# Kernel optimization log

Measured on AMD Instinct MI355X. Metric: run time of the kernel, lower is better.

The kernel has to match this reference:

```python
import jax, jax.numpy as jnp
import numpy as np

N_NODES = 50000
N_EDGES = 800000
D = 64
NUM_GRAPHS = 64


def gcn_conv(x, src, dst, deg_inv_sqrt, W, b):
    # GCNConv: h = X W; out_i = sum_{j->i} norm_ij * h_j + self-loop term + b
    h = x @ W  # [N, D_out]
    norm = deg_inv_sqrt[src] * deg_inv_sqrt[dst]  # [E]
    msgs = h[src] * norm[:, None]  # [E, D_out] -- dominant gather
    out = jax.ops.segment_sum(msgs, dst, num_segments=N_NODES)
    # self-loop edge (i,i) with norm = deg_i^-1
    out = out + h * (deg_inv_sqrt ** 2)[:, None]
    return out + b


def setup_inputs() -> dict:
    key = jax.random.key(0)
    ks = jax.random.split(key, 12)
    x = jax.random.normal(ks[0], (N_NODES, D), dtype=jnp.float32)
    edge_index = jax.random.randint(ks[1], (2, N_EDGES), 0, N_NODES, dtype=jnp.int64)
    batch = jnp.sort(jax.random.randint(ks[2], (N_NODES,), 0, NUM_GRAPHS, dtype=jnp.int64))
    s = 1.0 / np.sqrt(D)
    W1 = jax.random.uniform(ks[3], (D, D), jnp.float32, -s, s)
    b1 = jnp.zeros((D,), jnp.float32)
    W2 = jax.random.uniform(ks[4], (D, D), jnp.float32, -s, s)
    b2 = jnp.zeros((D,), jnp.float32)
    W3 = jax.random.uniform(ks[5], (D, D), jnp.float32, -s, s)
    b3 = jnp.zeros((D,), jnp.float32)
    Wl = jax.random.uniform(ks[6], (D, 1), jnp.float32, -s, s)
    bl = jnp.zeros((1,), jnp.float32)
    return {"x": x, "edge_index": edge_index, "batch": batch,
            "W1": W1, "b1": b1, "W2": W2, "b2": b2, "W3": W3, "b3": b3,
            "Wl": Wl, "bl": bl}


def reference(x, edge_index, batch, W1, b1, W2, b2, W3, b3, Wl, bl):
    src, dst = edge_index[0], edge_index[1]
    # symmetric GCN normalization with self-loops: deg_i = in_degree_i + 1
    deg = jax.ops.segment_sum(jnp.ones((N_EDGES,), x.dtype), dst, num_segments=N_NODES) + 1.0
    deg_inv_sqrt = deg ** -0.5
    h = jax.nn.relu(gcn_conv(x, src, dst, deg_inv_sqrt, W1, b1))
    h = jax.nn.relu(gcn_conv(h, src, dst, deg_inv_sqrt, W2, b2))
    h = jax.nn.relu(gcn_conv(h, src, dst, deg_inv_sqrt, W3, b3))
    # global mean pool over graphs
    sums = jax.ops.segment_sum(h, batch, num_segments=NUM_GRAPHS)  # [G, D]
    counts = jax.ops.segment_sum(jnp.ones((N_NODES,), h.dtype), batch, num_segments=NUM_GRAPHS)
    pooled = sums / jnp.clip(counts, 1.0)[:, None]
    return pooled @ Wl + bl  # [G, 1]
```

## Files before the change

kernel.cpp:

```cpp
#include <hip/hip_runtime.h>

#define N_NODES 50000
#define N_EDGES 800000
#define DIM 64
#define NUM_GRAPHS 64
#define NPART 8
#define PART_NODES 6250

typedef unsigned short u16;
typedef unsigned int u32;

__device__ __forceinline__ u16 bf16_rne(float f) {
  u32 u = __float_as_uint(f);
  u32 r = (u + 0x7fffu + ((u >> 16) & 1u)) >> 16;
  return (u16)r;
}

__global__ void init_kernel(int* __restrict__ cnt, float* __restrict__ partial,
                            const float* __restrict__ x, u16* __restrict__ xh) {
  int i = blockIdx.x * blockDim.x + threadIdx.x;
  if (i < N_NODES) cnt[i] = 0;
  if (i < NUM_GRAPHS) partial[i] = 0.f;
  int stride = gridDim.x * blockDim.x;
  for (int k = i; k < N_NODES * DIM / 4; k += stride) {
    float4 v = reinterpret_cast<const float4*>(x)[k];
    ushort4 o;
    o.x = bf16_rne(v.x); o.y = bf16_rne(v.y);
    o.z = bf16_rne(v.z); o.w = bf16_rne(v.w);
    reinterpret_cast<ushort4*>(xh)[k] = o;
  }
}

__global__ void count_deg_kernel(const int* __restrict__ dst, int* __restrict__ cnt, int E) {
  int stride = gridDim.x * blockDim.x;
  for (int e = blockIdx.x * blockDim.x + threadIdx.x; e < E; e += stride)
    atomicAdd(&cnt[dst[e]], 1);
}

__global__ void scanA_kernel(const int* __restrict__ cnt, int* __restrict__ rowptr,
                             int* __restrict__ bsum, float* __restrict__ dis, int N) {
  __shared__ int wsum[16];
  int i = blockIdx.x * 1024 + threadIdx.x;
  int lane = threadIdx.x & 63, wid = threadIdx.x >> 6;
  int v = (i < N) ? cnt[i] : 0;
  if (i < N) dis[i] = rsqrtf((float)(v + 1));
  int sv = v;
  #pragma unroll
  for (int off = 1; off < 64; off <<= 1) {
    int t = __shfl_up(sv, off, 64);
    if (lane >= off) sv += t;
  }
  if (lane == 63) wsum[wid] = sv;
  __syncthreads();
  if (wid == 0) {
    int wv = (lane < 16) ? wsum[lane] : 0;
    #pragma unroll
    for (int off = 1; off < 16; off <<= 1) {
      int t = __shfl_up(wv, off, 64);
      if (lane >= off) wv += t;
    }
    if (lane < 16) wsum[lane] = wv;
  }
  __syncthreads();
  if (i < N) rowptr[i] = (wid ? wsum[wid - 1] : 0) + (sv - v);
  if (threadIdx.x == 1023) bsum[blockIdx.x] = wsum[15];
}

__global__ void scanC_kernel(int* __restrict__ rowptr, const int* __restrict__ bsum,
                             int* __restrict__ cursor, int nb, int N) {
  __shared__ int s_off;
  __shared__ int s_total;
  int b = blockIdx.x;
  if (threadIdx.x < 64) {
    int t = threadIdx.x;
    int v = (t < nb) ? bsum[t] : 0;
    #pragma unroll
    for (int off = 1; off < 64; off <<= 1) {
      int u = __shfl_up(v, off, 64);
      if (t >= off) v += u;
    }
    if (t == (b == 0 ? 0 : b - 1)) s_off = (b == 0) ? 0 : v;
    if (t == nb - 1) s_total = v;
  }
  __syncthreads();
  int i = b * 1024 + threadIdx.x;
  if (i < N) {
    int r = rowptr[i] + s_off;
    rowptr[i] = r;
    cursor[i] = r;
  }
  if (b == 0 && threadIdx.x == 0) rowptr[N] = s_total;
}

__global__ void fill_kernel(const int* __restrict__ src, const int* __restrict__ dst,
                            const float* __restrict__ dis,
                            int* __restrict__ cursor, int2* __restrict__ epair, int E) {
  int p = blockIdx.x & 7;
  int lo = p * PART_NODES, hi = lo + PART_NODES;
  int stride = (gridDim.x >> 3) * blockDim.x;
  for (int e = (blockIdx.x >> 3) * blockDim.x + threadIdx.x; e < E; e += stride) {
    int d = dst[e];
    if (d >= lo && d < hi) {
      int s = src[e];
      int pos = atomicAdd(&cursor[d], 1);
      epair[pos] = make_int2(s, __float_as_int(dis[s]));
    }
  }
}

#define UNPACK_FMA(q, d)                                              \
  a0 = fmaf(__uint_as_float((q).x << 16), (d), a0);                   \
  a1 = fmaf(__uint_as_float((q).x & 0xffff0000u), (d), a1);           \
  a2 = fmaf(__uint_as_float((q).y << 16), (d), a2);                   \
  a3 = fmaf(__uint_as_float((q).y & 0xffff0000u), (d), a3);           \
  a4 = fmaf(__uint_as_float((q).z << 16), (d), a4);                   \
  a5 = fmaf(__uint_as_float((q).z & 0xffff0000u), (d), a5);           \
  a6 = fmaf(__uint_as_float((q).w << 16), (d), a6);                   \
  a7 = fmaf(__uint_as_float((q).w & 0xffff0000u), (d), a7);

__global__ __launch_bounds__(256) void aggregate_kernel(const u16* __restrict__ Fh,
    const int* __restrict__ rowptr, const int2* __restrict__ epair,
    const float* __restrict__ dis, float* __restrict__ A, int N) {
  int node = blockIdx.x * 4 + (threadIdx.x >> 6);
  if (node >= N) return;
  int lane = threadIdx.x & 63;
  int qc = lane & 7;
  int qe = lane >> 3;
  const uint4* __restrict__ F8 = reinterpret_cast<const uint4*>(Fh);
  int beg = rowptr[node], end = rowptr[node + 1];
  float a0 = 0.f, a1 = 0.f, a2 = 0.f, a3 = 0.f;
  float a4 = 0.f, a5 = 0.f, a6 = 0.f, a7 = 0.f;
  int j = beg;
  for (; j + 16 <= end; j += 16) {
    int2 p0 = epair[j + qe];
    int2 p1 = epair[j + 8 + qe];
    uint4 q0 = F8[(size_t)p0.x * 8 + qc];
    uint4 q1 = F8[(size_t)p1.x * 8 + qc];
    float d0 = __int_as_float(p0.y), d1 = __int_as_float(p1.y);
    UNPACK_FMA(q0, d0)
    UNPACK_FMA(q1, d1)
  }
  if (j + 8 <= end) {
    int2 p0 = epair[j + qe];
    uint4 q0 = F8[(size_t)p0.x * 8 + qc];
    float d0 = __int_as_float(p0.y);
    UNPACK_FMA(q0, d0)
    j += 8;
  }
  if (j + qe < end) {
    int2 p0 = epair[j + qe];
    uint4 q0 = F8[(size_t)p0.x * 8 + qc];
    float d0 = __int_as_float(p0.y);
    UNPACK_FMA(q0, d0)
  }
  #pragma unroll
  for (int m = 8; m < 64; m <<= 1) {
    a0 += __shfl_xor(a0, m, 64); a1 += __shfl_xor(a1, m, 64);
    a2 += __shfl_xor(a2, m, 64); a3 += __shfl_xor(a3, m, 64);
    a4 += __shfl_xor(a4, m, 64); a5 += __shfl_xor(a5, m, 64);
    a6 += __shfl_xor(a6, m, 64); a7 += __shfl_xor(a7, m, 64);
  }
  if (qe == 0) {
    float dn = dis[node];
    uint4 qs = F8[(size_t)node * 8 + qc];
    float s0 = __uint_as_float(qs.x << 16), s1 = __uint_as_float(qs.x & 0xffff0000u);
    float s2 = __uint_as_float(qs.y << 16), s3 = __uint_as_float(qs.y & 0xffff0000u);
    float s4 = __uint_as_float(qs.z << 16), s5 = __uint_as_float(qs.z & 0xffff0000u);
    float s6 = __uint_as_float(qs.w << 16), s7 = __uint_as_float(qs.w & 0xffff0000u);
    float4 o0, o1;
    o0.x = (a0 + s0 * dn) * dn; o0.y = (a1 + s1 * dn) * dn;
    o0.z = (a2 + s2 * dn) * dn; o0.w = (a3 + s3 * dn) * dn;
    o1.x = (a4 + s4 * dn) * dn; o1.y = (a5 + s5 * dn) * dn;
    o1.z = (a6 + s6 * dn) * dn; o1.w = (a7 + s7 * dn) * dn;
    float4* A4 = reinterpret_cast<float4*>(A + (size_t)node * DIM + qc * 8);
    A4[0] = o0;
    A4[1] = o1;
  }
}

__global__ __launch_bounds__(256) void gemm_bias_relu(const float* __restrict__ X,
    const float* __restrict__ W, const float* __restrict__ b,
    u16* __restrict__ Fh, int N) {
  __shared__ float4 Xs[64][16];
  int col = threadIdx.x & 63, wid = threadIdx.x >> 6;
  float wreg[DIM];
  #pragma unroll
  for (int k = 0; k < DIM; ++k) wreg[k] = W[k * DIM + col];
  float bias = b[col];
  int row0 = blockIdx.x * 64;
  for (int i = threadIdx.x; i < 64 * 16; i += 256) {
    int r = i >> 4, c = i & 15;
    int gr = row0 + r;
    Xs[r][c] = (gr < N) ? reinterpret_cast<const float4*>(X)[(size_t)gr * 16 + c]
                        : make_float4(0.f, 0.f, 0.f, 0.f);
  }
  __syncthreads();
  for (int rr = 0; rr < 16; ++rr) {
    int lr = wid * 16 + rr;
    int row = row0 + lr;
    if (row >= N) break;
    float a0 = 0.f, a1 = 0.f, a2 = 0.f, a3 = 0.f;
    #pragma unroll
    for (int kk = 0; kk < 16; ++kk) {
      float4 xv = Xs[lr][kk];
      a0 = fmaf(xv.x, wreg[4 * kk + 0], a0);
      a1 = fmaf(xv.y, wreg[4 * kk + 1], a1);
      a2 = fmaf(xv.z, wreg[4 * kk + 2], a2);
      a3 = fmaf(xv.w, wreg[4 * kk + 3], a3);
    }
    float v = fmaxf(a0 + a1 + a2 + a3 + bias, 0.f);
    Fh[(size_t)row * DIM + col] = bf16_rne(v);
  }
}

__global__ __launch_bounds__(256) void gemm_dot_kernel(const float* __restrict__ X,
    const float* __restrict__ W, const float* __restrict__ b, const float* __restrict__ Wl,
    const int* __restrict__ batch, float* __restrict__ partial, int N) {
  __shared__ float4 Xs[64][16];
  __shared__ float yv[64];
  __shared__ float gpart[NUM_GRAPHS];
  int col = threadIdx.x & 63, wid = threadIdx.x >> 6;
  float wreg[DIM];
  #pragma unroll
  for (int k = 0; k < DIM; ++k) wreg[k] = W[k * DIM + col];
  float bias = b[col];
  float wl = Wl[col];
  int row0 = blockIdx.x * 64;
  if (threadIdx.x < 64) { yv[threadIdx.x] = 0.f; gpart[threadIdx.x] = 0.f; }
  for (int i = threadIdx.x; i < 64 * 16; i += 256) {
    int r = i >> 4, c = i & 15;
    int gr = row0 + r;
    Xs[r][c] = (gr < N) ? reinterpret_cast<const float4*>(X)[(size_t)gr * 16 + c]
                        : make_float4(0.f, 0.f, 0.f, 0.f);
  }
  __syncthreads();
  for (int rr = 0; rr < 16; ++rr) {
    int lr = wid * 16 + rr;
    int row = row0 + lr;
    if (row >= N) break;
    float a0 = 0.f, a1 = 0.f, a2 = 0.f, a3 = 0.f;
    #pragma unroll
    for (int kk = 0; kk < 16; ++kk) {
      float4 xv = Xs[lr][kk];
      a0 = fmaf(xv.x, wreg[4 * kk + 0], a0);
      a1 = fmaf(xv.y, wreg[4 * kk + 1], a1);
      a2 = fmaf(xv.z, wreg[4 * kk + 2], a2);
      a3 = fmaf(xv.w, wreg[4 * kk + 3], a3);
    }
    float v = fmaxf(a0 + a1 + a2 + a3 + bias, 0.f);
    float y = v * wl;
    #pragma unroll
    for (int off = 32; off > 0; off >>= 1) y += __shfl_down(y, off, 64);
    if (col == 0) yv[lr] = y;
  }
  __syncthreads();
  if (threadIdx.x < 64) {
    int row = row0 + threadIdx.x;
    if (row < N) atomicAdd(&gpart[batch[row]], yv[threadIdx.x]);
  }
  __syncthreads();
  if (threadIdx.x < NUM_GRAPHS) {
    int glo = batch[row0];
    int ghi = batch[min(row0 + 63, N - 1)];
    int g = threadIdx.x;
    if (g >= glo && g <= ghi) atomicAdd(&partial[g], gpart[g]);
  }
}

__global__ void pool_final_kernel(const float* __restrict__ partial, const int* __restrict__ batch,
                                  const float* __restrict__ bl, float* __restrict__ out, int N) {
  int g = threadIdx.x;
  int lo = 0, hi = N;
  while (lo < hi) { int m = (lo + hi) >> 1; if (batch[m] < g) lo = m + 1; else hi = m; }
  int start = lo;
  hi = N;
  while (lo < hi) { int m = (lo + hi) >> 1; if (batch[m] < g + 1) lo = m + 1; else hi = m; }
  float c = fmaxf((float)(lo - start), 1.f);
  out[g] = partial[g] / c + bl[0];
}

extern "C" void kernel_launch(void* const* d_in, const int* in_sizes, int n_in,
                              void* d_out, int out_size, void* d_ws, size_t ws_size,
                              hipStream_t stream) {
  const float* x     = (const float*)d_in[0];
  const int*   ei    = (const int*)d_in[1];
  const int*   batch = (const int*)d_in[2];
  const float* W1 = (const float*)d_in[3];
  const float* b1 = (const float*)d_in[4];
  const float* W2 = (const float*)d_in[5];
  const float* b2 = (const float*)d_in[6];
  const float* W3 = (const float*)d_in[7];
  const float* b3 = (const float*)d_in[8];
  const float* Wl = (const float*)d_in[9];
  const float* bl = (const float*)d_in[10];
  float* out = (float*)d_out;

  const int* srcp = ei;
  const int* dstp = ei + N_EDGES;

  char* ws = (char*)d_ws;
  size_t off = 0;
  auto alloc = [&](size_t bytes) { void* p = ws + off; off += (bytes + 255) & ~(size_t)255; return p; };
  int*   cnt     = (int*)  alloc((size_t)N_NODES * 4);
  float* dis     = (float*)alloc((size_t)N_NODES * 4);
  int*   rowptr  = (int*)  alloc((size_t)(N_NODES + 1) * 4);
  int*   bsum    = (int*)  alloc(64 * 4);
  float* partial = (float*)alloc(NUM_GRAPHS * 4);
  int2*  epair   = (int2*) alloc((size_t)N_EDGES * 8);
  u16*   xh      = (u16*)  alloc((size_t)N_NODES * DIM * 2);
  u16*   fh      = (u16*)  alloc((size_t)N_NODES * DIM * 2);
  float* A       = (float*)alloc((size_t)N_NODES * DIM * 4);

  const int NB = (N_NODES + 1023) / 1024;

  init_kernel<<<(N_NODES + 255) / 256, 256, 0, stream>>>(cnt, partial, x, xh);
  count_deg_kernel<<<1024, 256, 0, stream>>>(dstp, cnt, N_EDGES);
  scanA_kernel<<<NB, 1024, 0, stream>>>(cnt, rowptr, bsum, dis, N_NODES);
  scanC_kernel<<<NB, 1024, 0, stream>>>(rowptr, bsum, cnt, NB, N_NODES);
  fill_kernel<<<1024, 256, 0, stream>>>(srcp, dstp, dis, cnt, epair, N_EDGES);

  const int GB = (N_NODES + 63) / 64;
  const int AB = (N_NODES + 3) / 4;
  aggregate_kernel<<<AB, 256, 0, stream>>>(xh, rowptr, epair, dis, A, N_NODES);
  gemm_bias_relu<<<GB, 256, 0, stream>>>(A, W1, b1, fh, N_NODES);
  aggregate_kernel<<<AB, 256, 0, stream>>>(fh, rowptr, epair, dis, A, N_NODES);
  gemm_bias_relu<<<GB, 256, 0, stream>>>(A, W2, b2, xh, N_NODES);
  aggregate_kernel<<<AB, 256, 0, stream>>>(xh, rowptr, epair, dis, A, N_NODES);
  gemm_dot_kernel<<<GB, 256, 0, stream>>>(A, W3, b3, Wl, batch, partial, N_NODES);
  pool_final_kernel<<<1, 64, 0, stream>>>(partial, batch, bl, out, N_NODES);
}
```

Before: 227.0 us.

## Fuse GCN aggregation with dense transform per layer and pool via per-node outputs

Each layer's neighbour aggregation and 64x64 GEMM + bias + ReLU now run in one kernel. The aggregated row goes into a per-wave shared-memory buffer and is multiplied by W held in LDS, so the fp32 intermediate matrix is never written to or read back from global memory. The last layer writes one scalar per node (the dot with Wl), and a per-graph block reduction replaces the atomic partial sums. In exchange every block of four nodes reloads the full 16KB weight matrix into LDS, which adds heavy L2 traffic and LDS pressure that may reduce occupancy.

New measurement: 240.7 us. 1.06x slower.

```diff
diff --git a/kernel.cpp b/kernel.cpp
--- a/kernel.cpp
+++ b/kernel.cpp
@@ -16,11 +16,10 @@
   return (u16)r;
 }
 
-__global__ void init_kernel(int* __restrict__ cnt, float* __restrict__ partial,
+__global__ void init_kernel(int* __restrict__ cnt,
                             const float* __restrict__ x, u16* __restrict__ xh) {
   int i = blockIdx.x * blockDim.x + threadIdx.x;
   if (i < N_NODES) cnt[i] = 0;
-  if (i < NUM_GRAPHS) partial[i] = 0.f;
   int stride = gridDim.x * blockDim.x;
   for (int k = i; k < N_NODES * DIM / 4; k += stride) {
     float4 v = reinterpret_cast<const float4*>(x)[k];
@@ -118,15 +117,30 @@
   a6 = fmaf(__uint_as_float((q).w << 16), (d), a6);                   \
   a7 = fmaf(__uint_as_float((q).w & 0xffff0000u), (d), a7);
 
-__global__ __launch_bounds__(256) void aggregate_kernel(const u16* __restrict__ Fh,
+template <int LAST>
+__global__ __launch_bounds__(256) void fused_layer(const u16* __restrict__ Fh,
     const int* __restrict__ rowptr, const int2* __restrict__ epair,
-    const float* __restrict__ dis, float* __restrict__ A, int N) {
-  int node = blockIdx.x * 4 + (threadIdx.x >> 6);
+    const float* __restrict__ dis, const float* __restrict__ W,
+    const float* __restrict__ b, u16* __restrict__ FhOut,
+    const float* __restrict__ Wl, float* __restrict__ ynode, int N) {
+  __shared__ float Ws[DIM][DIM];
+  __shared__ float rowbuf[4][DIM];
+
+  for (int i = threadIdx.x; i < DIM * DIM / 4; i += 256)
+    reinterpret_cast<float4*>(&Ws[0][0])[i] = reinterpret_cast<const float4*>(W)[i];
+  __syncthreads();
+
+  int lane = threadIdx.x & 63;
+  int wid = threadIdx.x >> 6;
+  int node = blockIdx.x * 4 + wid;
   if (node >= N) return;
-  int lane = threadIdx.x & 63;
   int qc = lane & 7;
   int qe = lane >> 3;
   const uint4* __restrict__ F8 = reinterpret_cast<const uint4*>(Fh);
+
+  float bias = b[lane];
+  float wl = LAST ? Wl[lane] : 0.f;
+
   int beg = rowptr[node], end = rowptr[node + 1];
   float a0 = 0.f, a1 = 0.f, a2 = 0.f, a3 = 0.f;
   float a4 = 0.f, a5 = 0.f, a6 = 0.f, a7 = 0.f;
@@ -172,111 +186,47 @@
     o0.z = (a2 + s2 * dn) * dn; o0.w = (a3 + s3 * dn) * dn;
     o1.x = (a4 + s4 * dn) * dn; o1.y = (a5 + s5 * dn) * dn;
     o1.z = (a6 + s6 * dn) * dn; o1.w = (a7 + s7 * dn) * dn;
-    float4* A4 = reinterpret_cast<float4*>(A + (size_t)node * DIM + qc * 8);
-    A4[0] = o0;
-    A4[1] = o1;
-  }
-}
-
-__global__ __launch_bounds__(256) void gemm_bias_relu(const float* __restrict__ X,
-    const float* __restrict__ W, const float* __restrict__ b,
-    u16* __restrict__ Fh, int N) {
-  __shared__ float4 Xs[64][16];
-  int col = threadIdx.x & 63, wid = threadIdx.x >> 6;
-  float wreg[DIM];
-  #pragma unroll
-  for (int k = 0; k < DIM; ++k) wreg[k] = W[k * DIM + col];
-  float bias = b[col];
-  int row0 = blockIdx.x * 64;
-  for (int i = threadIdx.x; i < 64 * 16; i += 256) {
-    int r = i >> 4, c = i & 15;
-    int gr = row0 + r;
-    Xs[r][c] = (gr < N) ? reinterpret_cast<const float4*>(X)[(size_t)gr * 16 + c]
-                        : make_float4(0.f, 0.f, 0.f, 0.f);
-  }
-  __syncthreads();
-  for (int rr = 0; rr < 16; ++rr) {
-    int lr = wid * 16 + rr;
-    int row = row0 + lr;
-    if (row >= N) break;
-    float a0 = 0.f, a1 = 0.f, a2 = 0.f, a3 = 0.f;
-    #pragma unroll
-    for (int kk = 0; kk < 16; ++kk) {
-      float4 xv = Xs[lr][kk];
-      a0 = fmaf(xv.x, wreg[4 * kk + 0], a0);
-      a1 = fmaf(xv.y, wreg[4 * kk + 1], a1);
-      a2 = fmaf(xv.z, wreg[4 * kk + 2], a2);
-      a3 = fmaf(xv.w, wreg[4 * kk + 3], a3);
-    }
-    float v = fmaxf(a0 + a1 + a2 + a3 + bias, 0.f);
-    Fh[(size_t)row * DIM + col] = bf16_rne(v);
-  }
-}
-
-__global__ __launch_bounds__(256) void gemm_dot_kernel(const float* __restrict__ X,
-    const float* __restrict__ W, const float* __restrict__ b, const float* __restrict__ Wl,
-    const int* __restrict__ batch, float* __restrict__ partial, int N) {
-  __shared__ float4 Xs[64][16];
-  __shared__ float yv[64];
-  __shared__ float gpart[NUM_GRAPHS];
-  int col = threadIdx.x & 63, wid = threadIdx.x >> 6;
-  float wreg[DIM];
-  #pragma unroll
-  for (int k = 0; k < DIM; ++k) wreg[k] = W[k * DIM + col];
-  float bias = b[col];
-  float wl = Wl[col];
-  int row0 = blockIdx.x * 64;
-  if (threadIdx.x < 64) { yv[threadIdx.x] = 0.f; gpart[threadIdx.x] = 0.f; }
-  for (int i = threadIdx.x; i < 64 * 16; i += 256) {
-    int r = i >> 4, c = i & 15;
-    int gr = row0 + r;
-    Xs[r][c] = (gr < N) ? reinterpret_cast<const float4*>(X)[(size_t)gr * 16 + c]
-                        : make_float4(0.f, 0.f, 0.f, 0.f);
-  }
-  __syncthreads();
-  for (int rr = 0; rr < 16; ++rr) {
-    int lr = wid * 16 + rr;
-    int row = row0 + lr;
-    if (row >= N) break;
-    float a0 = 0.f, a1 = 0.f, a2 = 0.f, a3 = 0.f;
-    #pragma unroll
-    for (int kk = 0; kk < 16; ++kk) {
-      float4 xv = Xs[lr][kk];
-      a0 = fmaf(xv.x, wreg[4 * kk + 0], a0);
-      a1 = fmaf(xv.y, wreg[4 * kk + 1], a1);
-      a2 = fmaf(xv.z, wreg[4 * kk + 2], a2);
-      a3 = fmaf(xv.w, wreg[4 * kk + 3], a3);
-    }
-    float v = fmaxf(a0 + a1 + a2 + a3 + bias, 0.f);
+    float4* rb = reinterpret_cast<float4*>(&rowbuf[wid][qc * 8]);
+    rb[0] = o0;
+    rb[1] = o1;
+  }
+  float acc = bias;
+  #pragma unroll 8
+  for (int k = 0; k < DIM; ++k)
+    acc = fmaf(rowbuf[wid][k], Ws[k][lane], acc);
+  float v = fmaxf(acc, 0.f);
+  if (!LAST) {
+    FhOut[(size_t)node * DIM + lane] = bf16_rne(v);
+  } else {
     float y = v * wl;
     #pragma unroll
     for (int off = 32; off > 0; off >>= 1) y += __shfl_down(y, off, 64);
-    if (col == 0) yv[lr] = y;
-  }
-  __syncthreads();
-  if (threadIdx.x < 64) {
-    int row = row0 + threadIdx.x;
-    if (row < N) atomicAdd(&gpart[batch[row]], yv[threadIdx.x]);
-  }
-  __syncthreads();
-  if (threadIdx.x < NUM_GRAPHS) {
-    int glo = batch[row0];
-    int ghi = batch[min(row0 + 63, N - 1)];
-    int g = threadIdx.x;
-    if (g >= glo && g <= ghi) atomicAdd(&partial[g], gpart[g]);
-  }
-}
-
-__global__ void pool_final_kernel(const float* __restrict__ partial, const int* __restrict__ batch,
+    if (lane == 0) ynode[node] = y;
+  }
+}
+
+__global__ void pool_final_kernel(const float* __restrict__ ynode, const int* __restrict__ batch,
                                   const float* __restrict__ bl, float* __restrict__ out, int N) {
-  int g = threadIdx.x;
+  __shared__ float wsums[4];
+  int g = blockIdx.x;
   int lo = 0, hi = N;
   while (lo < hi) { int m = (lo + hi) >> 1; if (batch[m] < g) lo = m + 1; else hi = m; }
   int start = lo;
   hi = N;
   while (lo < hi) { int m = (lo + hi) >> 1; if (batch[m] < g + 1) lo = m + 1; else hi = m; }
-  float c = fmaxf((float)(lo - start), 1.f);
-  out[g] = partial[g] / c + bl[0];
+  int end = lo;
+  float acc = 0.f;
+  for (int i = start + threadIdx.x; i < end; i += 256) acc += ynode[i];
+  #pragma unroll
+  for (int off = 32; off > 0; off >>= 1) acc += __shfl_down(acc, off, 64);
+  int lane = threadIdx.x & 63, wid = threadIdx.x >> 6;
+  if (lane == 0) wsums[wid] = acc;
+  __syncthreads();
+  if (threadIdx.x == 0) {
+    float s = wsums[0] + wsums[1] + wsums[2] + wsums[3];
+    float c = fmaxf((float)(end - start), 1.f);
+    out[g] = s / c + bl[0];
+  }
 }
 
 extern "C" void kernel_launch(void* const* d_in, const int* in_sizes, int n_in,
@@ -305,27 +255,25 @@
   float* dis     = (float*)alloc((size_t)N_NODES * 4);
   int*   rowptr  = (int*)  alloc((size_t)(N_NODES + 1) * 4);
   int*   bsum    = (int*)  alloc(64 * 4);
-  float* partial = (float*)alloc(NUM_GRAPHS * 4);
+  float* ynode   = (float*)alloc((size_t)N_NODES * 4);
   int2*  epair   = (int2*) alloc((size_t)N_EDGES * 8);
   u16*   xh      = (u16*)  alloc((size_t)N_NODES * DIM * 2);
   u16*   fh      = (u16*)  alloc((size_t)N_NODES * DIM * 2);
-  float* A       = (float*)alloc((size_t)N_NODES * DIM * 4);
 
   const int NB = (N_NODES + 1023) / 1024;
 
-  init_kernel<<<(N_NODES + 255) / 256, 256, 0, stream>>>(cnt, partial, x, xh);
+  init_kernel<<<(N_NODES + 255) / 256, 256, 0, stream>>>(cnt, x, xh);
   count_deg_kernel<<<1024, 256, 0, stream>>>(dstp, cnt, N_EDGES);
   scanA_kernel<<<NB, 1024, 0, stream>>>(cnt, rowptr, bsum, dis, N_NODES);
   scanC_kernel<<<NB, 1024, 0, stream>>>(rowptr, bsum, cnt, NB, N_NODES);
   fill_kernel<<<1024, 256, 0, stream>>>(srcp, dstp, dis, cnt, epair, N_EDGES);
 
-  const int GB = (N_NODES + 63) / 64;
   const int AB = (N_NODES + 3) / 4;
-  aggregate_kernel<<<AB, 256, 0, stream>>>(xh, rowptr, epair, dis, A, N_NODES);
-  gemm_bias_relu<<<GB, 256, 0, stream>>>(A, W1, b1, fh, N_NODES);
-  aggregate_kernel<<<AB, 256, 0, stream>>>(fh, rowptr, epair, dis, A, N_NODES);
-  gemm_bias_relu<<<GB, 256, 0, stream>>>(A, W2, b2, xh, N_NODES);
-  aggregate_kernel<<<AB, 256, 0, stream>>>(xh, rowptr, epair, dis, A, N_NODES);
-  gemm_dot_kernel<<<GB, 256, 0, stream>>>(A, W3, b3, Wl, batch, partial, N_NODES);
-  pool_final_kernel<<<1, 64, 0, stream>>>(partial, batch, bl, out, N_NODES);
-}
+  fused_layer<0><<<AB, 256, 0, stream>>>(xh, rowptr, epair, dis, W1, b1, fh,
+                                         nullptr, nullptr, N_NODES);
+  fused_layer<0><<<AB, 256, 0, stream>>>(fh, rowptr, epair, dis, W2, b2, xh,
+                                         nullptr, nullptr, N_NODES);
+  fused_layer<1><<<AB, 256, 0, stream>>>(xh, rowptr, epair, dis, W3, b3, nullptr,
+                                         Wl, ynode, N_NODES);
+  pool_final_kernel<<<NUM_GRAPHS, 256, 0, stream>>>(ynode, batch, bl, out, N_NODES);
+}
```
